# Kernel tuning notes

Hardware: AMD Instinct MI355X
Metric: run time of the kernel (lower is better)

The kernel has to match this reference:

```python
import jax, jax.numpy as jnp
import numpy as np

B, P, K = 8, 1024, 20  # clouds, points per cloud, kNN neighbors
OUT = 40
EPS = 1e-5


def leaky(x):
    return jnp.where(x >= 0, x, 0.2 * x)


def batch_norm(h, gamma, beta):
    mu = jnp.mean(h, axis=0)
    var = jnp.var(h, axis=0)
    return (h - mu) * jax.lax.rsqrt(var + EPS) * gamma + beta


def edge_conv(x, W, b, k):
    # x: [B,P,C]. Dynamic kNN in feature space (self included, as torch_cluster knn),
    # edge feature nn([x_i, x_j - x_i]) (single plain Linear per PyG MLP plain_last),
    # then max-aggregation over the k neighbors.
    sq = jnp.sum(x * x, axis=-1)                                  # [B,P]
    d = sq[:, :, None] + sq[:, None, :] - 2.0 * jnp.einsum('bpc,bqc->bpq', x, x)
    idx = jax.lax.top_k(-d, k)[1]                                  # [B,P,k]
    xj = jax.vmap(lambda xc, ic: xc[ic])(x, idx)                   # [B,P,k,C]
    xi = jnp.broadcast_to(x[:, :, None, :], xj.shape)
    e = jnp.concatenate([xi, xj - xi], axis=-1)                    # [B,P,k,2C]
    h = jnp.einsum('bpke,ec->bpkc', e, W) + b
    return jnp.max(h, axis=2)                                      # [B,P,Cout]


def setup_inputs() -> dict:
    key = jax.random.key(0)
    ks = jax.random.split(key, 16)
    s = 0.1
    pos = jax.random.normal(ks[0], (B * P, 3), dtype=jnp.float32)
    batch = jnp.repeat(jnp.arange(B, dtype=jnp.int32), P)
    return {
        'pos': pos, 'batch': batch,
        'W1': jax.random.normal(ks[1], (6, 64), jnp.float32) * s,    'b1': jnp.zeros((64,), jnp.float32),
        'W2': jax.random.normal(ks[2], (128, 64), jnp.float32) * s,  'b2': jnp.zeros((64,), jnp.float32),
        'W3': jax.random.normal(ks[3], (128, 128), jnp.float32) * s, 'b3': jnp.zeros((128,), jnp.float32),
        'W4': jax.random.normal(ks[4], (256, 256), jnp.float32) * s, 'b4': jnp.zeros((256,), jnp.float32),
        'Wm': jax.random.normal(ks[5], (512, 1024), jnp.float32) * s, 'bm': jnp.zeros((1024,), jnp.float32),
        'Wa': jax.random.normal(ks[6], (2048, 512), jnp.float32) * s, 'ba': jnp.zeros((512,), jnp.float32),
        'ga': jnp.ones((512,), jnp.float32),  'bea': jnp.zeros((512,), jnp.float32),
        'Wb': jax.random.normal(ks[7], (512, 256), jnp.float32) * s, 'bb': jnp.zeros((256,), jnp.float32),
        'gb': jnp.ones((256,), jnp.float32),  'beb': jnp.zeros((256,), jnp.float32),
        'Wc': jax.random.normal(ks[8], (256, OUT), jnp.float32) * s, 'bc': jnp.zeros((OUT,), jnp.float32),
    }


def reference(pos, batch, W1, b1, W2, b2, W3, b3, W4, b4, Wm, bm,
              Wa, ba, ga, bea, Wb, bb, gb, beb, Wc, bc):
    # batch ids are contiguous with P points per cloud -> reshape to [B,P,.]
    x = pos.reshape(B, P, 3)
    x1 = edge_conv(x, W1, b1, K)    # [B,P,64]
    x2 = edge_conv(x1, W2, b2, K)   # [B,P,64]
    x3 = edge_conv(x2, W3, b3, K)   # [B,P,128]
    x4 = edge_conv(x3, W4, b4, K)   # [B,P,256]
    cat = jnp.concatenate([x1, x2, x3, x4], axis=-1)  # [B,P,512]
    out = cat @ Wm + bm                                # [B,P,1024] (plain Linear)
    gmax = jnp.max(out, axis=1)                        # global_max_pool  [B,1024]
    gmean = jnp.mean(out, axis=1)                      # global_mean_pool [B,1024]
    h = jnp.concatenate([gmax, gmean], axis=-1)        # [B,2048]
    h = leaky(batch_norm(h @ Wa + ba, ga, bea))        # dropout = identity (eval)
    h = leaky(batch_norm(h @ Wb + bb, gb, beb))
    return h @ Wc + bc                                 # [B,40]
```

## Files before the change

kernel.cpp:

```cpp
#include <hip/hip_runtime.h>
#include <hip/hip_bf16.h>

#define NB 8
#define NP 1024
#define NPTS (NB * NP)
#define KNN 20

using bf16x8 = __attribute__((ext_vector_type(8))) short;
using f32x4 = __attribute__((ext_vector_type(4))) float;
using u64x16 = __attribute__((ext_vector_type(16))) unsigned long long;
using u32x16 = __attribute__((ext_vector_type(16))) unsigned int;

static __device__ __forceinline__ unsigned long long umin64(unsigned long long a,
                                                            unsigned long long b) {
    return a < b ? a : b;
}

static __device__ __forceinline__ void split_bf16(float v, unsigned short& h,
                                                  unsigned short& l) {
    __hip_bfloat16 hb = __float2bfloat16(v);
    float hf = __bfloat162float(hb);
    __hip_bfloat16 lb = __float2bfloat16(v - hf);
    h = *(unsigned short*)&hb;
    l = *(unsigned short*)&lb;
// ... 44 lines not shown
        if (r == KNN - 1) break;
        unsigned mlo = (unsigned)m;
#pragma unroll
        for (int j = 0; j < 16; ++j)
            if ((unsigned)k[j] == mlo) k[j] = ~0ull;
    }
}

static __device__ __forceinline__ void topk20_sel(u32x16 d, int lane,
                                                  unsigned long long* __restrict__ cand,
                                                  int* __restrict__ out) {
    unsigned lm = d[0];
#pragma unroll
    for (int j = 1; j < 16; ++j) lm = (d[j] < lm) ? d[j] : lm;
    unsigned srt = wave_bitonic_sort_u32(lm, lane);
    unsigned T = (unsigned)__shfl((int)srt, 19, 64);

    const unsigned long long below = (1ull << lane) - 1ull;
    int base = 0;
#pragma unroll
    for (int j = 0; j < 16; ++j) {
        bool sel = (d[j] <= T);
        unsigned long long mask = __ballot(sel);
        if (sel) {
            int pos = base + (int)__popcll(mask & below);
            if (pos < 64)
                cand[pos] = ((unsigned long long)d[j] << 32) | (unsigned)(j * 64 + lane);
        }
        base += (int)__popcll(mask);
    }

    if (base <= 64) {
        unsigned long long v = (lane < base) ? cand[lane] : ~0ull;
        unsigned hi = (unsigned)(v >> 32);
        unsigned hs = wave_bitonic_sort_u32(hi, lane);
        unsigned t2 = (unsigned)__shfl((int)hs, 19, 64);
        bool sel2 = (lane < base) && (hi <= t2);
        unsigned long long m2 = __ballot(sel2);
        if ((int)__popcll(m2) == KNN) {
            if (sel2) out[(int)__popcll(m2 & below)] = (int)(v & 0xffffffffu);
        } else {
            unsigned long long sv = wave_bitonic_sort(v, lane);
            if (lane < KNN) out[lane] = (int)(sv & 0xffffffffu);
        }
    } else {
        u64x16 k;
#pragma unroll
        for (int j = 0; j < 16; ++j)
            k[j] = ((unsigned long long)d[j] << 32) | (unsigned)(j * 64 + lane);
        topk20_wave(k, lane, out);
    }
}

__global__ __launch_bounds__(256) void knn3_kernel(const float* __restrict__ x,
                                                   int* __restrict__ idx) {
    const int w = threadIdx.x >> 6, lane = threadIdx.x & 63;
    const int p = blockIdx.x * 4 + w;
    const int b = p >> 10, pr = p & 1023;
    const int tid = threadIdx.x;
    __shared__ float sx[3][1024];
    __shared__ float ssq[1024];
    __shared__ unsigned long long cand[4][64];
    const float* xb = x + (size_t)b * NP * 3;

    for (int t = tid; t < 1024; t += 256) {
        float vx = xb[t * 3 + 0], vy = xb[t * 3 + 1], vz = xb[t * 3 + 2];
        sx[0][t] = vx;
        sx[1][t] = vy;
        sx[2][t] = vz;
        ssq[t] = vx * vx + vy * vy + vz * vz;
    }
    __syncthreads();

    const float px = sx[0][pr], py = sx[1][pr], pz = sx[2][pr];
    const float sqp = ssq[pr];

    u32x16 d;
#pragma unroll
    for (int j = 0; j < 16; ++j) {
        int q = j * 64 + lane;
        float dot = px * sx[0][q];
        dot += py * sx[1][q];
        dot += pz * sx[2][q];
        float dv = sqp + ssq[q] - 2.0f * dot;
        unsigned u = __float_as_uint(dv);
        d[j] = (u & 0x80000000u) ? ~u : (u | 0x80000000u);
    }
    topk20_sel(d, lane, cand[w], idx + (size_t)p * KNN);
}

template <int C>
__global__ __launch_bounds__(256) void sqnorm_kernel(const float* __restrict__ x,
                                                     float* __restrict__ sqn) {
    int p = blockIdx.x * 256 + threadIdx.x;
    if (p < NPTS) {
        const float* xp = x + (size_t)p * C;
        float s = 0.f;
        for (int c = 0; c < C; ++c) s += xp[c] * xp[c];
        sqn[p] = s;
    }
}

static __device__ __forceinline__ void pack_store(unsigned short h[8],
                                                  unsigned short l[8], size_t ci,
                                                  unsigned short* __restrict__ Wh,
                                                  unsigned short* __restrict__ Wl) {
    uint4 hp, lp;
    hp.x = h[0] | ((unsigned)h[1] << 16);
    hp.y = h[2] | ((unsigned)h[3] << 16);
    hp.z = h[4] | ((unsigned)h[5] << 16);
    hp.w = h[6] | ((unsigned)h[7] << 16);
    lp.x = l[0] | ((unsigned)l[1] << 16);
    lp.y = l[2] | ((unsigned)l[3] << 16);
    lp.z = l[4] | ((unsigned)l[5] << 16);
    lp.w = l[6] | ((unsigned)l[7] << 16);
    ((uint4*)Wh)[ci] = hp;
    ((uint4*)Wl)[ci] = lp;
}

static __device__ void conv_edge_w(const float* __restrict__ W, int Cin, int Cout,
                                   int g, unsigned short* __restrict__ Wh,
                                   unsigned short* __restrict__ Wl) {
    int N2 = 2 * Cout;
    if (g >= (Cin / 8) * N2) return;
    int n = g % N2, ks = g / N2;
    unsigned short h[8], l[8];
#pragma unroll
    for (int j = 0; j < 8; ++j) {
        int c = ks * 8 + j;
        float v;
        if (n < Cout)
            v = W[(size_t)c * Cout + n] - W[(size_t)(Cin + c) * Cout + n];
        else
            v = W[(size_t)(Cin + c) * Cout + (n - Cout)];
        split_bf16(v, h[j], l[j]);
    }
    pack_store(h, l, (size_t)ks * N2 + n, Wh, Wl);
}

__global__ __launch_bounds__(256) void convert_all_w_kernel(
        const float* __restrict__ Wm, const float* __restrict__ W2,
        const float* __restrict__ W3, const float* __restrict__ W4,
        unsigned short* __restrict__ Wmh, unsigned short* __restrict__ Wml,
        unsigned short* __restrict__ W2h, unsigned short* __restrict__ W2l,
        unsigned short* __restrict__ W3h, unsigned short* __restrict__ W3l,
        unsigned short* __restrict__ W4h, unsigned short* __restrict__ W4l) {
    int bid = blockIdx.x;
    if (bid < 256) {
        int g = bid * 256 + threadIdx.x;
        int n = g & 1023, ks = g >> 10;
        unsigned short h[8], l[8];
#pragma unroll
        for (int j = 0; j < 8; ++j) {
            float v = Wm[(size_t)(ks * 8 + j) * 1024 + n];
            split_bf16(v, h[j], l[j]);
        }
        pack_store(h, l, (size_t)ks * 1024 + n, Wmh, Wml);
    } else if (bid < 288) {
        conv_edge_w(W4, 128, 256, (bid - 256) * 256 + threadIdx.x, W4h, W4l);
    } else if (bid < 296) {
        conv_edge_w(W3, 64, 128, (bid - 288) * 256 + threadIdx.x, W3h, W3l);
    } else {
        conv_edge_w(W2, 64, 64, (bid - 296) * 256 + threadIdx.x, W2h, W2l);
    }
}

template <int C>
__global__ __launch_bounds__(256, 2) void knn_mfma_kernel(
        const unsigned short* __restrict__ Xhp, const unsigned short* __restrict__ Xlp,
        const float* __restrict__ sqn, int* __restrict__ idx) {
    constexpr int NCK = C / 32;
    const int bid = blockIdx.x;
    const int b = bid >> 6, rg = bid & 63;
    const int g0 = b * NP;
    const int p0 = rg * 16;
    const int tid = threadIdx.x;
    const int wid = tid >> 6, lane = tid & 63;
    const int fkb = lane >> 4, flm = lane & 15;

    __shared__ float sD[16][1028];
    __shared__ float sqa[16];
    __shared__ float sqb[1024];
    __shared__ unsigned long long cand[4][64];

    if (tid < 16) sqa[tid] = sqn[g0 + p0 + tid];
    for (int t = tid; t < 1024; t += 256) sqb[t] = sqn[g0 + t];
    __syncthreads();

    const uint4* Ah4 = (const uint4*)Xhp;
    const uint4* Al4 = (const uint4*)Xlp;

    uint4 fAh[NCK], fAl[NCK];
#pragma unroll
    for (int kk = 0; kk < NCK; ++kk) {
        size_t a = (size_t)(4 * kk + fkb) * NPTS + g0 + p0 + flm;
        fAh[kk] = Ah4[a];
        fAl[kk] = Al4[a];
    }

    const int r4 = fkb * 4, cc = flm;

#pragma unroll
    for (int t = 0; t < 2; ++t) {
        const int c0 = (wid + t * 4) * 128;
        f32x4 acc[8];
#pragma unroll
        for (int j = 0; j < 8; ++j) acc[j] = {0.f, 0.f, 0.f, 0.f};

#pragma unroll
        for (int kk = 0; kk < NCK; ++kk) {
            uint4 fBh[8], fBl[8];
#pragma unroll
            for (int j = 0; j < 8; ++j) {
                size_t bi = (size_t)(4 * kk + fkb) * NPTS + g0 + c0 + j * 16 + flm;
                fBh[j] = Ah4[bi];
                fBl[j] = Al4[bi];
            }
            bf16x8 ah = *(const bf16x8*)&fAh[kk];
            bf16x8 al = *(const bf16x8*)&fAl[kk];
#pragma unroll
            for (int j = 0; j < 8; ++j) {
                bf16x8 bh = *(const bf16x8*)&fBh[j];
                bf16x8 bl = *(const bf16x8*)&fBl[j];
                acc[j] = __builtin_amdgcn_mfma_f32_16x16x32_bf16(ah, bh, acc[j], 0, 0, 0);
                acc[j] = __builtin_amdgcn_mfma_f32_16x16x32_bf16(ah, bl, acc[j], 0, 0, 0);
                acc[j] = __builtin_amdgcn_mfma_f32_16x16x32_bf16(al, bh, acc[j], 0, 0, 0);
            }
        }

#pragma unroll
        for (int r = 0; r < 4; ++r) {
            int row = r4 + r;
            float sp = sqa[row];
#pragma unroll
            for (int j = 0; j < 8; ++j) {
                int col = c0 + j * 16 + cc;
                sD[row][col] = sp + sqb[col] - 2.0f * acc[j][r];
            }
        }
    }
    __syncthreads();

    for (int rr = 0; rr < 4; ++rr) {
        int row = wid * 4 + rr;
        u32x16 d;
#pragma unroll
        for (int j = 0; j < 16; ++j) {
            int q = j * 64 + lane;
            unsigned u = __float_as_uint(sD[row][q]);
            d[j] = (u & 0x80000000u) ? ~u : (u | 0x80000000u);
        }
        topk20_sel(d, lane, cand[wid], idx + (size_t)(g0 + p0 + row) * KNN);
    }
}

template <int Cin, int Cout>
__global__ __launch_bounds__(256, 2) void edge_mfma_kernel(
        const unsigned short* __restrict__ Xhp, const unsigned short* __restrict__ Xlp,
        const unsigned short* __restrict__ Whp, const unsigned short* __restrict__ Wlp,
        const float* __restrict__ bias, float* __restrict__ AB) {
    constexpr int N2 = 2 * Cout;
    constexpr int NCK = Cin / 32;
    const int n0 = blockIdx.x * 128;
    const int p0 = blockIdx.y * 128;
    const int tid = threadIdx.x;
    const int wid = tid >> 6, lane = tid & 63;
    const int wm = (wid >> 1) * 64, wn = (wid & 1) * 64;

    __shared__ uint4 sAh[2][4][132], sAl[2][4][132], sBh[2][4][132], sBl[2][4][132];

    f32x4 acc[4][4];
#pragma unroll
    for (int i = 0; i < 4; ++i)
#pragma unroll
        for (int j = 0; j < 4; ++j) acc[i][j] = {0.f, 0.f, 0.f, 0.f};

    const uint4* Ah4 = (const uint4*)Xhp;
    const uint4* Al4 = (const uint4*)Xlp;
    const uint4* Wh4 = (const uint4*)Whp;
    const uint4* Wl4 = (const uint4*)Wlp;

    const int m0 = tid & 127, kb0 = tid >> 7;
    uint4 rAh0, rAl0, rBh0, rBl0, rAh1, rAl1, rBh1, rBl1;

#define EM_LOAD(ck)                                                     \
    {                                                                   \
        int ksb = (ck) * 4;                                             \
        size_t a0 = (size_t)(ksb + kb0) * NPTS + p0 + m0;               \
        size_t a1 = (size_t)(ksb + kb0 + 2) * NPTS + p0 + m0;           \
        size_t b0 = (size_t)(ksb + kb0) * N2 + n0 + m0;                 \
        size_t b1 = (size_t)(ksb + kb0 + 2) * N2 + n0 + m0;             \
        rAh0 = Ah4[a0]; rAl0 = Al4[a0];                                 \
        rAh1 = Ah4[a1]; rAl1 = Al4[a1];                                 \
        rBh0 = Wh4[b0]; rBl0 = Wl4[b0];                                 \
        rBh1 = Wh4[b1]; rBl1 = Wl4[b1];                                 \
    }

#define EM_WRITE(buf)                                                   \
    {                                                                   \
        sAh[buf][kb0][m0] = rAh0;  sAl[buf][kb0][m0] = rAl0;            \
        sAh[buf][kb0 + 2][m0] = rAh1;  sAl[buf][kb0 + 2][m0] = rAl1;    \
        sBh[buf][kb0][m0] = rBh0;  sBl[buf][kb0][m0] = rBl0;            \
        sBh[buf][kb0 + 2][m0] = rBh1;  sBl[buf][kb0 + 2][m0] = rBl1;    \
    }

    EM_LOAD(0);
    EM_WRITE(0);
    __syncthreads();

    const int fkb = lane >> 4, flm = lane & 15;

    for (int ck = 0; ck < NCK; ++ck) {
        const int buf = ck & 1;
        if (ck < NCK - 1) EM_LOAD(ck + 1);

        bf16x8 fAh[4], fAl[4], fBh[4], fBl[4];
#pragma unroll
        for (int i = 0; i < 4; ++i) {
            fAh[i] = *(const bf16x8*)&sAh[buf][fkb][wm + i * 16 + flm];
            fAl[i] = *(const bf16x8*)&sAl[buf][fkb][wm + i * 16 + flm];
            fBh[i] = *(const bf16x8*)&sBh[buf][fkb][wn + i * 16 + flm];
            fBl[i] = *(const bf16x8*)&sBl[buf][fkb][wn + i * 16 + flm];
        }
#pragma unroll
        for (int i = 0; i < 4; ++i)
#pragma unroll
            for (int j = 0; j < 4; ++j) {
                acc[i][j] = __builtin_amdgcn_mfma_f32_16x16x32_bf16(fAh[i], fBh[j],
                                                                    acc[i][j], 0, 0, 0);
                acc[i][j] = __builtin_amdgcn_mfma_f32_16x16x32_bf16(fAh[i], fBl[j],
                                                                    acc[i][j], 0, 0, 0);
                acc[i][j] = __builtin_amdgcn_mfma_f32_16x16x32_bf16(fAl[i], fBh[j],
                                                                    acc[i][j], 0, 0, 0);
            }

        if (ck < NCK - 1) EM_WRITE(buf ^ 1);
        __syncthreads();
    }

    const int r4 = (lane >> 4) * 4, cc = lane & 15;
    float bj[4];
#pragma unroll
    for (int j = 0; j < 4; ++j) {
        int cg = n0 + wn + j * 16 + cc;
        bj[j] = (cg < Cout) ? bias[cg] : 0.f;
    }
#pragma unroll
    for (int i = 0; i < 4; ++i) {
#pragma unroll
        for (int r = 0; r < 4; ++r) {
            int row = wm + i * 16 + r4 + r;
            float* orow = AB + (size_t)(p0 + row) * N2 + n0;
#pragma unroll
            for (int j = 0; j < 4; ++j)
                orow[wn + j * 16 + cc] = acc[i][j][r] + bj[j];
        }
    }
#undef EM_LOAD
#undef EM_WRITE
}

template <int Cin, int Cout>
__global__ __launch_bounds__(256) void edge_gemm_kernel(const float* __restrict__ x,
                                                        const float* __restrict__ W,
                                                        const float* __restrict__ bias,
                                                        float* __restrict__ AB) {
    constexpr int N2 = 2 * Cout;
    constexpr int BK = (Cin < 32) ? Cin : 32;
    const int n0 = blockIdx.x * 128;
    const int p0 = blockIdx.y * 64;
    const int tid = threadIdx.x;
    const int tx = tid & 15, ty = tid >> 4;

    __shared__ float sX[BK][68];
    __shared__ float sW[BK][132];

    float acc[4][8];
#pragma unroll
    for (int i = 0; i < 4; ++i)
#pragma unroll
        for (int j = 0; j < 8; ++j) acc[i][j] = 0.f;

    for (int k0 = 0; k0 < Cin; k0 += BK) {
        for (int t = tid; t < 64 * BK; t += 256) {
            int m = t / BK, c = t - m * BK;
            sX[c][m] = x[(size_t)(p0 + m) * Cin + c];
        }
        for (int t = tid; t < BK * 128; t += 256) {
            int c = t >> 7, n = t & 127;
            int nn = n0 + n;
            float w;
            if (nn < Cout)
                w = W[(size_t)(k0 + c) * Cout + nn] - W[(size_t)(Cin + k0 + c) * Cout + nn];
            else
                w = W[(size_t)(Cin + k0 + c) * Cout + (nn - Cout)];
            sW[c][n] = w;
        }
        __syncthreads();

#pragma unroll
        for (int c = 0; c < BK; ++c) {
            float4 a4 = *(const float4*)&sX[c][ty * 4];
            float4 w0 = *(const float4*)&sW[c][tx * 4];
            float4 w1 = *(const float4*)&sW[c][64 + tx * 4];
            float av[4] = {a4.x, a4.y, a4.z, a4.w};
#pragma unroll
            for (int i = 0; i < 4; ++i) {
                acc[i][0] += av[i] * w0.x;
                acc[i][1] += av[i] * w0.y;
                acc[i][2] += av[i] * w0.z;
                acc[i][3] += av[i] * w0.w;
                acc[i][4] += av[i] * w1.x;
                acc[i][5] += av[i] * w1.y;
                acc[i][6] += av[i] * w1.z;
                acc[i][7] += av[i] * w1.w;
            }
        }
        __syncthreads();
    }

    const bool aH0 = (n0 < Cout);
    const bool aH1 = (n0 + 64 < Cout);
    float4 z4 = {0.f, 0.f, 0.f, 0.f};
    float4 bb0 = aH0 ? *(const float4*)&bias[n0 + tx * 4] : z4;
    float4 bb1 = aH1 ? *(const float4*)&bias[n0 + 64 + tx * 4] : z4;

#pragma unroll
    for (int i = 0; i < 4; ++i) {
        float* orow = AB + (size_t)(p0 + ty * 4 + i) * N2 + n0;
        float4 o0, o1;
        o0.x = acc[i][0] + bb0.x;
        o0.y = acc[i][1] + bb0.y;
        o0.z = acc[i][2] + bb0.z;
        o0.w = acc[i][3] + bb0.w;
        o1.x = acc[i][4] + bb1.x;
        o1.y = acc[i][5] + bb1.y;
        o1.z = acc[i][6] + bb1.z;
        o1.w = acc[i][7] + bb1.w;
        *(float4*)&orow[tx * 4] = o0;
        *(float4*)&orow[64 + tx * 4] = o1;
    }
}

template <int Cout>
__global__ __launch_bounds__(256) void gather_max_panel_kernel(
        const float* __restrict__ AB, const int* __restrict__ idx,
        float* __restrict__ y, unsigned short* __restrict__ Xh,
        unsigned short* __restrict__ Xl) {
    constexpr int N2 = 2 * Cout;
    constexpr int TPP = Cout / 4;
    constexpr int PPB = 256 / TPP;
    constexpr int RS = N2 / 4;
    const int pp = threadIdx.x / TPP;
    const int t = threadIdx.x % TPP;
    const int p = blockIdx.x * PPB + pp;
    const int base = p & ~(NP - 1);

    __shared__ int s_idx[PPB][KNN];
    for (int tt = threadIdx.x; tt < PPB * KNN; tt += 256) {
        int a = tt / KNN, r = tt - a * KNN;
        s_idx[a][r] = idx[(size_t)(blockIdx.x * PPB + a) * KNN + r];
    }
    __syncthreads();

    const float4* Brow = (const float4*)(AB + (size_t)base * N2 + Cout);

    int q0 = s_idx[pp][0];
    float4 m = Brow[(size_t)q0 * RS + t];
#pragma unroll
    for (int j = 1; j < KNN; ++j) {
        int q = s_idx[pp][j];
        float4 v = Brow[(size_t)q * RS + t];
        m.x = fmaxf(m.x, v.x);
        m.y = fmaxf(m.y, v.y);
        m.z = fmaxf(m.z, v.z);
        m.w = fmaxf(m.w, v.w);
    }
    float4 a = *(const float4*)(AB + (size_t)p * N2 + 4 * t);
    float4 o;
    o.x = a.x + m.x;
    o.y = a.y + m.y;
    o.z = a.z + m.z;
    o.w = a.w + m.w;
    *(float4*)(y + (size_t)p * Cout + 4 * t) = o;

    unsigned short h[4], l[4];
    split_bf16(o.x, h[0], l[0]);
    split_bf16(o.y, h[1], l[1]);
    split_bf16(o.z, h[2], l[2]);
    split_bf16(o.w, h[3], l[3]);
    const int ks = t >> 1;
    size_t u2 = ((size_t)ks * NPTS + p) * 2 + (t & 1);
    uint2 hp, lp;
    hp.x = h[0] | ((unsigned)h[1] << 16);
    hp.y = h[2] | ((unsigned)h[3] << 16);
    lp.x = l[0] | ((unsigned)l[1] << 16);
    lp.y = l[2] | ((unsigned)l[3] << 16);
    ((uint2*)Xh)[u2] = hp;
    ((uint2*)Xl)[u2] = lp;
}

__global__ __launch_bounds__(256) void catmean_kernel(
        const float* __restrict__ x1, const float* __restrict__ x2,
        const float* __restrict__ x3, const float* __restrict__ x4,
        float* __restrict__ catmean) {
    const int n0 = blockIdx.x * 128;
    const int b = blockIdx.y;
    const int tid = threadIdx.x;
    const int col = n0 + (tid & 127);
    const int half = tid >> 7;
    __shared__ float sred[256];

    const float* src;
    int cw, coff;
    if (col < 64) { src = x1; cw = 64; coff = col; }
    else if (col < 128) { src = x2; cw = 64; coff = col - 64; }
    else if (col < 256) { src = x3; cw = 128; coff = col - 128; }
    else { src = x4; cw = 256; coff = col - 256; }

    float s = 0.f;
    const float* base = src + ((size_t)b * NP + half * 512) * cw + coff;
    for (int p = 0; p < 512; ++p) s += base[(size_t)p * cw];
    sred[tid] = s;
    __syncthreads();
    if (tid < 128)
        catmean[(size_t)b * 512 + col] = (sred[tid] + sred[tid + 128]) * (1.0f / 1024.0f);
}

__global__ __launch_bounds__(256) void gmean_kernel(const float* __restrict__ catmean,
                                                    const float* __restrict__ Wm,
                                                    const float* __restrict__ bm,
                                                    float* __restrict__ gmeanv) {
    const int n0 = blockIdx.x * 128;
    const int b = blockIdx.y;
    const int tid = threadIdx.x;
    const int cg = tid & 31, kp = tid >> 5;
    const int col = n0 + cg * 4;
    __shared__ float4 part[8][32];

    float4 acc = {0.f, 0.f, 0.f, 0.f};
    for (int k = kp * 64; k < kp * 64 + 64; ++k) {
        float g = catmean[(size_t)b * 512 + k];
        float4 w = *(const float4*)&Wm[(size_t)k * 1024 + col];
        acc.x += g * w.x;
        acc.y += g * w.y;
        acc.z += g * w.z;
        acc.w += g * w.w;
    }
    part[kp][cg] = acc;
    __syncthreads();
    if (tid < 32) {
        float4 s = part[0][tid];
// ... 284 lines not shown
    const float* Wa = (const float*)d_in[12];
    const float* ba = (const float*)d_in[13];
    const float* ga = (const float*)d_in[14];
    const float* bea = (const float*)d_in[15];
    const float* Wb = (const float*)d_in[16];
    const float* bb = (const float*)d_in[17];
    const float* gb = (const float*)d_in[18];
    const float* beb = (const float*)d_in[19];
    const float* Wc = (const float*)d_in[20];
    const float* bc = (const float*)d_in[21];
    float* out = (float*)d_out;

    char* ws = (char*)d_ws;
    size_t off = 0;
    auto alloc = [&](size_t bytes) {
        void* p = ws + off;
        off += (bytes + 255) & ~(size_t)255;
        return p;
    };
    int* idx = (int*)alloc((size_t)NPTS * KNN * 4);
    float* x1 = (float*)alloc((size_t)NPTS * 64 * 4);
    float* x2 = (float*)alloc((size_t)NPTS * 64 * 4);
    float* x3 = (float*)alloc((size_t)NPTS * 128 * 4);
    float* x4 = (float*)alloc((size_t)NPTS * 256 * 4);
    float* scratch = (float*)alloc((size_t)NPTS * 512 * 4);
    float* pmax = (float*)alloc((size_t)64 * 1024 * 4);
    float* catmean = (float*)alloc(NB * 512 * 4);
    float* gmeanv = (float*)alloc(NB * 1024 * 4);
    float* ha = (float*)alloc(NB * 512 * 4);
    float* hb = (float*)alloc(NB * 256 * 4);
    float* sqn = (float*)alloc(NPTS * 4);
    unsigned short* Ach = (unsigned short*)alloc((size_t)64 * NPTS * 8 * 2);
    unsigned short* Acl = (unsigned short*)alloc((size_t)64 * NPTS * 8 * 2);
    unsigned short* Wth = (unsigned short*)alloc((size_t)64 * 1024 * 8 * 2);
    unsigned short* Wtl = (unsigned short*)alloc((size_t)64 * 1024 * 8 * 2);
    unsigned short* W2h = (unsigned short*)alloc((size_t)8 * 128 * 8 * 2);
    unsigned short* W2l = (unsigned short*)alloc((size_t)8 * 128 * 8 * 2);
    unsigned short* W3h = (unsigned short*)alloc((size_t)8 * 256 * 8 * 2);
    unsigned short* W3l = (unsigned short*)alloc((size_t)8 * 256 * 8 * 2);
    unsigned short* W4h = (unsigned short*)alloc((size_t)16 * 512 * 8 * 2);
    unsigned short* W4l = (unsigned short*)alloc((size_t)16 * 512 * 8 * 2);
    (void)ws_size;

    float* AB = scratch;
    const size_t REG = (size_t)NPTS * 8;
    unsigned short* x1h = Ach, *x1l = Acl;
    unsigned short* x2h = Ach + 8 * REG, *x2l = Acl + 8 * REG;
    unsigned short* x3h = Ach + 16 * REG, *x3l = Acl + 16 * REG;
    unsigned short* x4h = Ach + 32 * REG, *x4l = Acl + 32 * REG;

    convert_all_w_kernel<<<300, 256, 0, stream>>>(Wm, W2, W3, W4, Wth, Wtl, W2h, W2l,
                                                  W3h, W3l, W4h, W4l);

    knn3_kernel<<<NPTS / 4, 256, 0, stream>>>(pos, idx);
    edge_gemm_kernel<3, 64><<<dim3(1, 128), 256, 0, stream>>>(pos, W1, b1, AB);
    gather_max_panel_kernel<64><<<NPTS / 16, 256, 0, stream>>>(AB, idx, x1, x1h, x1l);

    sqnorm_kernel<64><<<NPTS / 256, 256, 0, stream>>>(x1, sqn);
    knn_mfma_kernel<64><<<512, 256, 0, stream>>>(x1h, x1l, sqn, idx);
    edge_mfma_kernel<64, 64><<<dim3(1, 64), 256, 0, stream>>>(x1h, x1l, W2h, W2l, b2, AB);
    gather_max_panel_kernel<64><<<NPTS / 16, 256, 0, stream>>>(AB, idx, x2, x2h, x2l);

    sqnorm_kernel<64><<<NPTS / 256, 256, 0, stream>>>(x2, sqn);
    knn_mfma_kernel<64><<<512, 256, 0, stream>>>(x2h, x2l, sqn, idx);
    edge_mfma_kernel<64, 128><<<dim3(2, 64), 256, 0, stream>>>(x2h, x2l, W3h, W3l, b3, AB);
    gather_max_panel_kernel<128><<<NPTS / 8, 256, 0, stream>>>(AB, idx, x3, x3h, x3l);

    sqnorm_kernel<128><<<NPTS / 256, 256, 0, stream>>>(x3, sqn);
    knn_mfma_kernel<128><<<512, 256, 0, stream>>>(x3h, x3l, sqn, idx);
    edge_mfma_kernel<128, 256><<<dim3(4, 64), 256, 0, stream>>>(x3h, x3l, W4h, W4l, b4, AB);
    gather_max_panel_kernel<256><<<NPTS / 4, 256, 0, stream>>>(AB, idx, x4, x4h, x4l);

    catmean_kernel<<<dim3(4, NB), 256, 0, stream>>>(x1, x2, x3, x4, catmean);
    gmean_kernel<<<dim3(8, NB), 256, 0, stream>>>(catmean, Wm, bm, gmeanv);

    gemm_cat_pool_kernel<<<512, 256, 0, stream>>>(Ach, Acl, Wth, Wtl, pmax);

    fc_a_kernel<<<dim3(8, NB), 256, 0, stream>>>(pmax, gmeanv, bm, Wa, ba, ha);
    fc_b_bn_kernel<<<dim3(4, NB), 256, 0, stream>>>(ha, ga, bea, Wb, bb, hb);
    fc_c_bn_kernel<<<2, 256, 0, stream>>>(hb, gb, beb, Wc, bc, out);
}
```

Baseline: 241.6 us.

## Fuse kNN and edge GEMM per layer into one launch, fold sqnorm into gather

Merges each layer's kNN kernel and its independent edge projection GEMM into a single launch, with block ID ranges picking the role and a shared-memory union between the two. The layer-1 kNN now handles 16 points per block instead of 4. The separate squared-norm kernels are folded into the gather-max kernel, which writes the norms from a shared row buffer. This removes several launches and lets the two independent workloads overlap on the GPU. The cost is a larger shared-memory footprint for the GEMM blocks and an extra barrier plus a serial per-point norm loop in the gather.

```diff
diff --git a/kernel.cpp b/kernel.cpp
--- a/kernel.cpp
+++ b/kernel.cpp
@@ -120,52 +120,397 @@
     }
 }
 
-__global__ __launch_bounds__(256) void knn3_kernel(const float* __restrict__ x,
-                                                   int* __restrict__ idx) {
-    const int w = threadIdx.x >> 6, lane = threadIdx.x & 63;
-    const int p = blockIdx.x * 4 + w;
-    const int b = p >> 10, pr = p & 1023;
+struct Knn3Shared {
+    float sx[3][1024];
+    float ssq[1024];
+    unsigned long long cand[4][64];
+};
+struct Edge1Shared {
+    float sX[3][68];
+    float sW[3][132];
+};
+union L1Shared {
+    Knn3Shared k;
+    Edge1Shared e;
+};
+
+struct KnnShared {
+    float sD[16][1028];
+    float sqa[16];
+    float sqb[1024];
+    unsigned long long cand[4][64];
+};
+struct EdgeShared {
+    uint4 sAh[2][4][132];
+    uint4 sAl[2][4][132];
+    uint4 sBh[2][4][132];
+    uint4 sBl[2][4][132];
+};
+union LayerShared {
+    KnnShared k;
+    EdgeShared e;
+};
+
+__global__ __launch_bounds__(256) void knn3_edge_kernel(const float* __restrict__ x,
+                                                        const float* __restrict__ W,
+                                                        const float* __restrict__ bias,
+                                                        int* __restrict__ idx,
+                                                        float* __restrict__ AB) {
+    __shared__ L1Shared su;
+    const int bid = blockIdx.x;
     const int tid = threadIdx.x;
-    __shared__ float sx[3][1024];
-    __shared__ float ssq[1024];
-    __shared__ unsigned long long cand[4][64];
-    const float* xb = x + (size_t)b * NP * 3;
-
-    for (int t = tid; t < 1024; t += 256) {
-        float vx = xb[t * 3 + 0], vy = xb[t * 3 + 1], vz = xb[t * 3 + 2];
-        sx[0][t] = vx;
-        sx[1][t] = vy;
-        sx[2][t] = vz;
-        ssq[t] = vx * vx + vy * vy + vz * vz;
-    }
-    __syncthreads();
-
-    const float px = sx[0][pr], py = sx[1][pr], pz = sx[2][pr];
-    const float sqp = ssq[pr];
-
-    u32x16 d;
-#pragma unroll
-    for (int j = 0; j < 16; ++j) {
-        int q = j * 64 + lane;
-        float dot = px * sx[0][q];
-        dot += py * sx[1][q];
-        dot += pz * sx[2][q];
-        float dv = sqp + ssq[q] - 2.0f * dot;
-        unsigned u = __float_as_uint(dv);
-        d[j] = (u & 0x80000000u) ? ~u : (u | 0x80000000u);
-    }
-    topk20_sel(d, lane, cand[w], idx + (size_t)p * KNN);
-}
-
-template <int C>
-__global__ __launch_bounds__(256) void sqnorm_kernel(const float* __restrict__ x,
-                                                     float* __restrict__ sqn) {
-    int p = blockIdx.x * 256 + threadIdx.x;
-    if (p < NPTS) {
-        const float* xp = x + (size_t)p * C;
-        float s = 0.f;
-        for (int c = 0; c < C; ++c) s += xp[c] * xp[c];
-        sqn[p] = s;
+
+    if (bid < 512) {
+        Knn3Shared& S = su.k;
+        const int wid = tid >> 6, lane = tid & 63;
+        const int b = bid >> 6, p0 = (bid & 63) * 16;
+        const int g0 = b * NP;
+        const float* xb = x + (size_t)g0 * 3;
+
+        for (int t = tid; t < 1024; t += 256) {
+            float vx = xb[t * 3 + 0], vy = xb[t * 3 + 1], vz = xb[t * 3 + 2];
+            S.sx[0][t] = vx;
+            S.sx[1][t] = vy;
+            S.sx[2][t] = vz;
+            S.ssq[t] = vx * vx + vy * vy + vz * vz;
+        }
+        __syncthreads();
+
+        for (int rr = 0; rr < 4; ++rr) {
+            int pr = p0 + wid * 4 + rr;
+            const float px = S.sx[0][pr], py = S.sx[1][pr], pz = S.sx[2][pr];
+            const float sqp = S.ssq[pr];
+            u32x16 d;
+#pragma unroll
+            for (int j = 0; j < 16; ++j) {
+                int q = j * 64 + lane;
+                float dot = px * S.sx[0][q];
+                dot += py * S.sx[1][q];
+                dot += pz * S.sx[2][q];
+                float dv = sqp + S.ssq[q] - 2.0f * dot;
+                unsigned u = __float_as_uint(dv);
+                d[j] = (u & 0x80000000u) ? ~u : (u | 0x80000000u);
+            }
+            topk20_sel(d, lane, S.cand[wid], idx + (size_t)(g0 + pr) * KNN);
+        }
+    } else {
+        Edge1Shared& S = su.e;
+        constexpr int Cin = 3, Cout = 64, N2 = 128;
+        const int p0 = (bid - 512) * 64;
+        const int tx = tid & 15, ty = tid >> 4;
+
+        for (int t = tid; t < 64 * Cin; t += 256) {
+            int m = t / Cin, c = t - m * Cin;
+            S.sX[c][m] = x[(size_t)(p0 + m) * Cin + c];
+        }
+        for (int t = tid; t < Cin * 128; t += 256) {
+            int c = t >> 7, n = t & 127;
+            float w;
+            if (n < Cout)
+                w = W[(size_t)c * Cout + n] - W[(size_t)(Cin + c) * Cout + n];
+            else
+                w = W[(size_t)(Cin + c) * Cout + (n - Cout)];
+            S.sW[c][n] = w;
+        }
+        __syncthreads();
+
+        float acc[4][8];
+#pragma unroll
+        for (int i = 0; i < 4; ++i)
+#pragma unroll
+            for (int j = 0; j < 8; ++j) acc[i][j] = 0.f;
+
+#pragma unroll
+        for (int c = 0; c < Cin; ++c) {
+            float4 a4 = *(const float4*)&S.sX[c][ty * 4];
+            float4 w0 = *(const float4*)&S.sW[c][tx * 4];
+            float4 w1 = *(const float4*)&S.sW[c][64 + tx * 4];
+            float av[4] = {a4.x, a4.y, a4.z, a4.w};
+#pragma unroll
+            for (int i = 0; i < 4; ++i) {
+                acc[i][0] += av[i] * w0.x;
+                acc[i][1] += av[i] * w0.y;
+                acc[i][2] += av[i] * w0.z;
+                acc[i][3] += av[i] * w0.w;
+                acc[i][4] += av[i] * w1.x;
+                acc[i][5] += av[i] * w1.y;
+                acc[i][6] += av[i] * w1.z;
+                acc[i][7] += av[i] * w1.w;
+            }
+        }
+
+        float4 bb0 = *(const float4*)&bias[tx * 4];
+#pragma unroll
+        for (int i = 0; i < 4; ++i) {
+            float* orow = AB + (size_t)(p0 + ty * 4 + i) * N2;
+            float4 o0, o1;
+            o0.x = acc[i][0] + bb0.x;
+            o0.y = acc[i][1] + bb0.y;
+            o0.z = acc[i][2] + bb0.z;
+            o0.w = acc[i][3] + bb0.w;
+            o1.x = acc[i][4];
+            o1.y = acc[i][5];
+            o1.z = acc[i][6];
+            o1.w = acc[i][7];
+            *(float4*)&orow[tx * 4] = o0;
+            *(float4*)&orow[64 + tx * 4] = o1;
+        }
+    }
+}
+
+template <int C, int Cout>
+__global__ __launch_bounds__(256, 2) void layer_kernel(
+        const unsigned short* __restrict__ Xhp, const unsigned short* __restrict__ Xlp,
+        const float* __restrict__ sqn, int* __restrict__ idx,
+        const unsigned short* __restrict__ Whp, const unsigned short* __restrict__ Wlp,
+        const float* __restrict__ bias, float* __restrict__ AB) {
+    __shared__ LayerShared su;
+    constexpr int NCK = C / 32;
+    const int bid = blockIdx.x;
+    const int tid = threadIdx.x;
+    const int wid = tid >> 6, lane = tid & 63;
+    const int fkb = lane >> 4, flm = lane & 15;
+    const uint4* Ah4 = (const uint4*)Xhp;
+    const uint4* Al4 = (const uint4*)Xlp;
+
+    if (bid < 512) {
+        KnnShared& S = su.k;
+        const int b = bid >> 6, rg = bid & 63;
+        const int g0 = b * NP;
+        const int p0 = rg * 16;
+
+        if (tid < 16) S.sqa[tid] = sqn[g0 + p0 + tid];
+        for (int t = tid; t < 1024; t += 256) S.sqb[t] = sqn[g0 + t];
+        __syncthreads();
+
+        uint4 fAh[NCK], fAl[NCK];
+#pragma unroll
+        for (int kk = 0; kk < NCK; ++kk) {
+            size_t a = (size_t)(4 * kk + fkb) * NPTS + g0 + p0 + flm;
+            fAh[kk] = Ah4[a];
+            fAl[kk] = Al4[a];
+        }
+
+        const int r4 = fkb * 4, cc = flm;
+
+#pragma unroll
+        for (int t = 0; t < 2; ++t) {
+            const int c0 = (wid + t * 4) * 128;
+            f32x4 acc[8];
+#pragma unroll
+            for (int j = 0; j < 8; ++j) acc[j] = {0.f, 0.f, 0.f, 0.f};
+
+#pragma unroll
+            for (int kk = 0; kk < NCK; ++kk) {
+                uint4 fBh[8], fBl[8];
+#pragma unroll
+                for (int j = 0; j < 8; ++j) {
+                    size_t bi = (size_t)(4 * kk + fkb) * NPTS + g0 + c0 + j * 16 + flm;
+                    fBh[j] = Ah4[bi];
+                    fBl[j] = Al4[bi];
+                }
+                bf16x8 ah = *(const bf16x8*)&fAh[kk];
+                bf16x8 al = *(const bf16x8*)&fAl[kk];
+#pragma unroll
+                for (int j = 0; j < 8; ++j) {
+                    bf16x8 bh = *(const bf16x8*)&fBh[j];
+                    bf16x8 bl = *(const bf16x8*)&fBl[j];
+                    acc[j] = __builtin_amdgcn_mfma_f32_16x16x32_bf16(ah, bh, acc[j], 0, 0, 0);
+                    acc[j] = __builtin_amdgcn_mfma_f32_16x16x32_bf16(ah, bl, acc[j], 0, 0, 0);
+                    acc[j] = __builtin_amdgcn_mfma_f32_16x16x32_bf16(al, bh, acc[j], 0, 0, 0);
+                }
+            }
+
+#pragma unroll
+            for (int r = 0; r < 4; ++r) {
+                int row = r4 + r;
+                float sp = S.sqa[row];
+#pragma unroll
+                for (int j = 0; j < 8; ++j) {
+                    int col = c0 + j * 16 + cc;
+                    S.sD[row][col] = sp + S.sqb[col] - 2.0f * acc[j][r];
+                }
+            }
+        }
+        __syncthreads();
+
+        for (int rr = 0; rr < 4; ++rr) {
+            int row = wid * 4 + rr;
+            u32x16 d;
+#pragma unroll
+            for (int j = 0; j < 16; ++j) {
+                int q = j * 64 + lane;
+                unsigned u = __float_as_uint(S.sD[row][q]);
+                d[j] = (u & 0x80000000u) ? ~u : (u | 0x80000000u);
+            }
+            topk20_sel(d, lane, S.cand[wid], idx + (size_t)(g0 + p0 + row) * KNN);
+        }
+    } else {
+        EdgeShared& S = su.e;
+        constexpr int N2 = 2 * Cout;
+        constexpr int NX = N2 / 128;
+        const int eb = bid - 512;
+        const int n0 = (eb % NX) * 128;
+        const int p0 = (eb / NX) * 128;
+        const int wm = (wid >> 1) * 64, wn = (wid & 1) * 64;
+
+        f32x4 acc[4][4];
+#pragma unroll
+        for (int i = 0; i < 4; ++i)
+#pragma unroll
+            for (int j = 0; j < 4; ++j) acc[i][j] = {0.f, 0.f, 0.f, 0.f};
+
+        const uint4* Wh4 = (const uint4*)Whp;
+        const uint4* Wl4 = (const uint4*)Wlp;
+
+        const int m0 = tid & 127, kb0 = tid >> 7;
+        uint4 rAh0, rAl0, rBh0, rBl0, rAh1, rAl1, rBh1, rBl1;
+
+#define EM_LOAD(ck)                                                     \
+    {                                                                   \
+        int ksb = (ck) * 4;                                             \
+        size_t a0 = (size_t)(ksb + kb0) * NPTS + p0 + m0;               \
+        size_t a1 = (size_t)(ksb + kb0 + 2) * NPTS + p0 + m0;           \
+        size_t b0 = (size_t)(ksb + kb0) * N2 + n0 + m0;                 \
+        size_t b1 = (size_t)(ksb + kb0 + 2) * N2 + n0 + m0;             \
+        rAh0 = Ah4[a0]; rAl0 = Al4[a0];                                 \
+        rAh1 = Ah4[a1]; rAl1 = Al4[a1];                                 \
+        rBh0 = Wh4[b0]; rBl0 = Wl4[b0];                                 \
+        rBh1 = Wh4[b1]; rBl1 = Wl4[b1];                                 \
+    }
+
+#define EM_WRITE(buf)                                                         \
+    {                                                                         \
+        S.sAh[buf][kb0][m0] = rAh0;  S.sAl[buf][kb0][m0] = rAl0;              \
+        S.sAh[buf][kb0 + 2][m0] = rAh1;  S.sAl[buf][kb0 + 2][m0] = rAl1;      \
+        S.sBh[buf][kb0][m0] = rBh0;  S.sBl[buf][kb0][m0] = rBl0;              \
+        S.sBh[buf][kb0 + 2][m0] = rBh1;  S.sBl[buf][kb0 + 2][m0] = rBl1;      \
+    }
+
+        EM_LOAD(0);
+        EM_WRITE(0);
+        __syncthreads();
+
+        for (int ck = 0; ck < NCK; ++ck) {
+            const int buf = ck & 1;
+            if (ck < NCK - 1) EM_LOAD(ck + 1);
+
+            bf16x8 fAh[4], fAl[4], fBh[4], fBl[4];
+#pragma unroll
+            for (int i = 0; i < 4; ++i) {
+                fAh[i] = *(const bf16x8*)&S.sAh[buf][fkb][wm + i * 16 + flm];
+                fAl[i] = *(const bf16x8*)&S.sAl[buf][fkb][wm + i * 16 + flm];
+                fBh[i] = *(const bf16x8*)&S.sBh[buf][fkb][wn + i * 16 + flm];
+                fBl[i] = *(const bf16x8*)&S.sBl[buf][fkb][wn + i * 16 + flm];
+            }
+#pragma unroll
+            for (int i = 0; i < 4; ++i)
+#pragma unroll
+                for (int j = 0; j < 4; ++j) {
+                    acc[i][j] = __builtin_amdgcn_mfma_f32_16x16x32_bf16(
+                            fAh[i], fBh[j], acc[i][j], 0, 0, 0);
+                    acc[i][j] = __builtin_amdgcn_mfma_f32_16x16x32_bf16(
+                            fAh[i], fBl[j], acc[i][j], 0, 0, 0);
+                    acc[i][j] = __builtin_amdgcn_mfma_f32_16x16x32_bf16(
+                            fAl[i], fBh[j], acc[i][j], 0, 0, 0);
+                }
+
+            if (ck < NCK - 1) EM_WRITE(buf ^ 1);
+            __syncthreads();
+        }
+
+        const int r4 = (lane >> 4) * 4, cc = lane & 15;
+        float bj[4];
+#pragma unroll
+        for (int j = 0; j < 4; ++j) {
+            int cg = n0 + wn + j * 16 + cc;
+            bj[j] = (cg < Cout) ? bias[cg] : 0.f;
+        }
+#pragma unroll
+        for (int i = 0; i < 4; ++i) {
+#pragma unroll
+            for (int r = 0; r < 4; ++r) {
+                int row = wm + i * 16 + r4 + r;
+                float* orow = AB + (size_t)(p0 + row) * N2 + n0;
+#pragma unroll
+                for (int j = 0; j < 4; ++j)
+                    orow[wn + j * 16 + cc] = acc[i][j][r] + bj[j];
+            }
+        }
+#undef EM_LOAD
+#undef EM_WRITE
+    }
+}
+
+template <int Cout, bool WSQ>
+__global__ __launch_bounds__(256) void gather_max_panel_kernel(
+        const float* __restrict__ AB, const int* __restrict__ idx,
+        float* __restrict__ y, unsigned short* __restrict__ Xh,
+        unsigned short* __restrict__ Xl, float* __restrict__ sqn) {
+    constexpr int N2 = 2 * Cout;
+    constexpr int TPP = Cout / 4;
+    constexpr int PPB = 256 / TPP;
+    constexpr int RS = N2 / 4;
+    const int pp = threadIdx.x / TPP;
+    const int t = threadIdx.x % TPP;
+    const int p = blockIdx.x * PPB + pp;
+    const int base = p & ~(NP - 1);
+
+    __shared__ int s_idx[PPB][KNN];
+    __shared__ float srow[PPB][Cout];
+    for (int tt = threadIdx.x; tt < PPB * KNN; tt += 256) {
+        int a = tt / KNN, r = tt - a * KNN;
+        s_idx[a][r] = idx[(size_t)(blockIdx.x * PPB + a) * KNN + r];
+    }
+    __syncthreads();
+
+    const float4* Brow = (const float4*)(AB + (size_t)base * N2 + Cout);
+
+    int q0 = s_idx[pp][0];
+    float4 m = Brow[(size_t)q0 * RS + t];
+#pragma unroll
+    for (int j = 1; j < KNN; ++j) {
+        int q = s_idx[pp][j];
+        float4 v = Brow[(size_t)q * RS + t];
+        m.x = fmaxf(m.x, v.x);
+        m.y = fmaxf(m.y, v.y);
+        m.z = fmaxf(m.z, v.z);
+        m.w = fmaxf(m.w, v.w);
+    }
+    float4 a = *(const float4*)(AB + (size_t)p * N2 + 4 * t);
+    float4 o;
+    o.x = a.x + m.x;
+    o.y = a.y + m.y;
+    o.z = a.z + m.z;
+    o.w = a.w + m.w;
+    *(float4*)(y + (size_t)p * Cout + 4 * t) = o;
+
+    unsigned short h[4], l[4];
+    split_bf16(o.x, h[0], l[0]);
+    split_bf16(o.y, h[1], l[1]);
+    split_bf16(o.z, h[2], l[2]);
+    split_bf16(o.w, h[3], l[3]);
+    const int ks = t >> 1;
+    size_t u2 = ((size_t)ks * NPTS + p) * 2 + (t & 1);
+    uint2 hp, lp;
+    hp.x = h[0] | ((unsigned)h[1] << 16);
+    hp.y = h[2] | ((unsigned)h[3] << 16);
+    lp.x = l[0] | ((unsigned)l[1] << 16);
+    lp.y = l[2] | ((unsigned)l[3] << 16);
+    ((uint2*)Xh)[u2] = hp;
+    ((uint2*)Xl)[u2] = lp;
+
+    if constexpr (WSQ) {
+        *(float4*)&srow[pp][4 * t] = o;
+        __syncthreads();
+        if (t == 0) {
+            float s = 0.f;
+            for (int c = 0; c < Cout; ++c) {
+                float v = srow[pp][c];
+                s += v * v;
+            }
+            sqn[p] = s;
+        }
     }
 }
 
@@ -231,341 +576,6 @@
     } else {
         conv_edge_w(W2, 64, 64, (bid - 296) * 256 + threadIdx.x, W2h, W2l);
     }
-}
-
-template <int C>
-__global__ __launch_bounds__(256, 2) void knn_mfma_kernel(
-        const unsigned short* __restrict__ Xhp, const unsigned short* __restrict__ Xlp,
-        const float* __restrict__ sqn, int* __restrict__ idx) {
-    constexpr int NCK = C / 32;
-    const int bid = blockIdx.x;
-    const int b = bid >> 6, rg = bid & 63;
-    const int g0 = b * NP;
-    const int p0 = rg * 16;
-    const int tid = threadIdx.x;
-    const int wid = tid >> 6, lane = tid & 63;
-    const int fkb = lane >> 4, flm = lane & 15;
-
-    __shared__ float sD[16][1028];
-    __shared__ float sqa[16];
-    __shared__ float sqb[1024];
-    __shared__ unsigned long long cand[4][64];
-
-    if (tid < 16) sqa[tid] = sqn[g0 + p0 + tid];
-    for (int t = tid; t < 1024; t += 256) sqb[t] = sqn[g0 + t];
-    __syncthreads();
-
-    const uint4* Ah4 = (const uint4*)Xhp;
-    const uint4* Al4 = (const uint4*)Xlp;
-
-    uint4 fAh[NCK], fAl[NCK];
-#pragma unroll
-    for (int kk = 0; kk < NCK; ++kk) {
-        size_t a = (size_t)(4 * kk + fkb) * NPTS + g0 + p0 + flm;
-        fAh[kk] = Ah4[a];
-        fAl[kk] = Al4[a];
-    }
-
-    const int r4 = fkb * 4, cc = flm;
-
-#pragma unroll
-    for (int t = 0; t < 2; ++t) {
-        const int c0 = (wid + t * 4) * 128;
-        f32x4 acc[8];
-#pragma unroll
-        for (int j = 0; j < 8; ++j) acc[j] = {0.f, 0.f, 0.f, 0.f};
-
-#pragma unroll
-        for (int kk = 0; kk < NCK; ++kk) {
-            uint4 fBh[8], fBl[8];
-#pragma unroll
-            for (int j = 0; j < 8; ++j) {
-                size_t bi = (size_t)(4 * kk + fkb) * NPTS + g0 + c0 + j * 16 + flm;
-                fBh[j] = Ah4[bi];
-                fBl[j] = Al4[bi];
-            }
-            bf16x8 ah = *(const bf16x8*)&fAh[kk];
-            bf16x8 al = *(const bf16x8*)&fAl[kk];
-#pragma unroll
-            for (int j = 0; j < 8; ++j) {
-                bf16x8 bh = *(const bf16x8*)&fBh[j];
-                bf16x8 bl = *(const bf16x8*)&fBl[j];
-                acc[j] = __builtin_amdgcn_mfma_f32_16x16x32_bf16(ah, bh, acc[j], 0, 0, 0);
-                acc[j] = __builtin_amdgcn_mfma_f32_16x16x32_bf16(ah, bl, acc[j], 0, 0, 0);
-                acc[j] = __builtin_amdgcn_mfma_f32_16x16x32_bf16(al, bh, acc[j], 0, 0, 0);
-            }
-        }
-
-#pragma unroll
-        for (int r = 0; r < 4; ++r) {
-            int row = r4 + r;
-            float sp = sqa[row];
-#pragma unroll
-            for (int j = 0; j < 8; ++j) {
-                int col = c0 + j * 16 + cc;
-                sD[row][col] = sp + sqb[col] - 2.0f * acc[j][r];
-            }
-        }
-    }
-    __syncthreads();
-
-    for (int rr = 0; rr < 4; ++rr) {
-        int row = wid * 4 + rr;
-        u32x16 d;
-#pragma unroll
-        for (int j = 0; j < 16; ++j) {
-            int q = j * 64 + lane;
-            unsigned u = __float_as_uint(sD[row][q]);
-            d[j] = (u & 0x80000000u) ? ~u : (u | 0x80000000u);
-        }
-        topk20_sel(d, lane, cand[wid], idx + (size_t)(g0 + p0 + row) * KNN);
-    }
-}
-
-template <int Cin, int Cout>
-__global__ __launch_bounds__(256, 2) void edge_mfma_kernel(
-        const unsigned short* __restrict__ Xhp, const unsigned short* __restrict__ Xlp,
-        const unsigned short* __restrict__ Whp, const unsigned short* __restrict__ Wlp,
-        const float* __restrict__ bias, float* __restrict__ AB) {
-    constexpr int N2 = 2 * Cout;
-    constexpr int NCK = Cin / 32;
-    const int n0 = blockIdx.x * 128;
-    const int p0 = blockIdx.y * 128;
-    const int tid = threadIdx.x;
-    const int wid = tid >> 6, lane = tid & 63;
-    const int wm = (wid >> 1) * 64, wn = (wid & 1) * 64;
-
-    __shared__ uint4 sAh[2][4][132], sAl[2][4][132], sBh[2][4][132], sBl[2][4][132];
-
-    f32x4 acc[4][4];
-#pragma unroll
-    for (int i = 0; i < 4; ++i)
-#pragma unroll
-        for (int j = 0; j < 4; ++j) acc[i][j] = {0.f, 0.f, 0.f, 0.f};
-
-    const uint4* Ah4 = (const uint4*)Xhp;
-    const uint4* Al4 = (const uint4*)Xlp;
-    const uint4* Wh4 = (const uint4*)Whp;
-    const uint4* Wl4 = (const uint4*)Wlp;
-
-    const int m0 = tid & 127, kb0 = tid >> 7;
-    uint4 rAh0, rAl0, rBh0, rBl0, rAh1, rAl1, rBh1, rBl1;
-
-#define EM_LOAD(ck)                                                     \
-    {                                                                   \
-        int ksb = (ck) * 4;                                             \
-        size_t a0 = (size_t)(ksb + kb0) * NPTS + p0 + m0;               \
-        size_t a1 = (size_t)(ksb + kb0 + 2) * NPTS + p0 + m0;           \
-        size_t b0 = (size_t)(ksb + kb0) * N2 + n0 + m0;                 \
-        size_t b1 = (size_t)(ksb + kb0 + 2) * N2 + n0 + m0;             \
-        rAh0 = Ah4[a0]; rAl0 = Al4[a0];                                 \
-        rAh1 = Ah4[a1]; rAl1 = Al4[a1];                                 \
-        rBh0 = Wh4[b0]; rBl0 = Wl4[b0];                                 \
-        rBh1 = Wh4[b1]; rBl1 = Wl4[b1];                                 \
-    }
-
-#define EM_WRITE(buf)                                                   \
-    {                                                                   \
-        sAh[buf][kb0][m0] = rAh0;  sAl[buf][kb0][m0] = rAl0;            \
-        sAh[buf][kb0 + 2][m0] = rAh1;  sAl[buf][kb0 + 2][m0] = rAl1;    \
-        sBh[buf][kb0][m0] = rBh0;  sBl[buf][kb0][m0] = rBl0;            \
-        sBh[buf][kb0 + 2][m0] = rBh1;  sBl[buf][kb0 + 2][m0] = rBl1;    \
-    }
-
-    EM_LOAD(0);
-    EM_WRITE(0);
-    __syncthreads();
-
-    const int fkb = lane >> 4, flm = lane & 15;
-
-    for (int ck = 0; ck < NCK; ++ck) {
-        const int buf = ck & 1;
-        if (ck < NCK - 1) EM_LOAD(ck + 1);
-
-        bf16x8 fAh[4], fAl[4], fBh[4], fBl[4];
-#pragma unroll
-        for (int i = 0; i < 4; ++i) {
-            fAh[i] = *(const bf16x8*)&sAh[buf][fkb][wm + i * 16 + flm];
-            fAl[i] = *(const bf16x8*)&sAl[buf][fkb][wm + i * 16 + flm];
-            fBh[i] = *(const bf16x8*)&sBh[buf][fkb][wn + i * 16 + flm];
-            fBl[i] = *(const bf16x8*)&sBl[buf][fkb][wn + i * 16 + flm];
-        }
-#pragma unroll
-        for (int i = 0; i < 4; ++i)
-#pragma unroll
-            for (int j = 0; j < 4; ++j) {
-                acc[i][j] = __builtin_amdgcn_mfma_f32_16x16x32_bf16(fAh[i], fBh[j],
-                                                                    acc[i][j], 0, 0, 0);
-                acc[i][j] = __builtin_amdgcn_mfma_f32_16x16x32_bf16(fAh[i], fBl[j],
-                                                                    acc[i][j], 0, 0, 0);
-                acc[i][j] = __builtin_amdgcn_mfma_f32_16x16x32_bf16(fAl[i], fBh[j],
-                                                                    acc[i][j], 0, 0, 0);
-            }
-
-        if (ck < NCK - 1) EM_WRITE(buf ^ 1);
-        __syncthreads();
-    }
-
-    const int r4 = (lane >> 4) * 4, cc = lane & 15;
-    float bj[4];
-#pragma unroll
-    for (int j = 0; j < 4; ++j) {
-        int cg = n0 + wn + j * 16 + cc;
-        bj[j] = (cg < Cout) ? bias[cg] : 0.f;
-    }
-#pragma unroll
-    for (int i = 0; i < 4; ++i) {
-#pragma unroll
-        for (int r = 0; r < 4; ++r) {
-            int row = wm + i * 16 + r4 + r;
-            float* orow = AB + (size_t)(p0 + row) * N2 + n0;
-#pragma unroll
-            for (int j = 0; j < 4; ++j)
-                orow[wn + j * 16 + cc] = acc[i][j][r] + bj[j];
-        }
-    }
-#undef EM_LOAD
-#undef EM_WRITE
-}
-
-template <int Cin, int Cout>
-__global__ __launch_bounds__(256) void edge_gemm_kernel(const float* __restrict__ x,
-                                                        const float* __restrict__ W,
-                                                        const float* __restrict__ bias,
-                                                        float* __restrict__ AB) {
-    constexpr int N2 = 2 * Cout;
-    constexpr int BK = (Cin < 32) ? Cin : 32;
-    const int n0 = blockIdx.x * 128;
-    const int p0 = blockIdx.y * 64;
-    const int tid = threadIdx.x;
-    const int tx = tid & 15, ty = tid >> 4;
-
-    __shared__ float sX[BK][68];
-    __shared__ float sW[BK][132];
-
-    float acc[4][8];
-#pragma unroll
-    for (int i = 0; i < 4; ++i)
-#pragma unroll
-        for (int j = 0; j < 8; ++j) acc[i][j] = 0.f;
-
-    for (int k0 = 0; k0 < Cin; k0 += BK) {
-        for (int t = tid; t < 64 * BK; t += 256) {
-            int m = t / BK, c = t - m * BK;
-            sX[c][m] = x[(size_t)(p0 + m) * Cin + c];
-        }
-        for (int t = tid; t < BK * 128; t += 256) {
-            int c = t >> 7, n = t & 127;
-            int nn = n0 + n;
-            float w;
-            if (nn < Cout)
-                w = W[(size_t)(k0 + c) * Cout + nn] - W[(size_t)(Cin + k0 + c) * Cout + nn];
-            else
-                w = W[(size_t)(Cin + k0 + c) * Cout + (nn - Cout)];
-            sW[c][n] = w;
-        }
-        __syncthreads();
-
-#pragma unroll
-        for (int c = 0; c < BK; ++c) {
-            float4 a4 = *(const float4*)&sX[c][ty * 4];
-            float4 w0 = *(const float4*)&sW[c][tx * 4];
-            float4 w1 = *(const float4*)&sW[c][64 + tx * 4];
-            float av[4] = {a4.x, a4.y, a4.z, a4.w};
-#pragma unroll
-            for (int i = 0; i < 4; ++i) {
-                acc[i][0] += av[i] * w0.x;
-                acc[i][1] += av[i] * w0.y;
-                acc[i][2] += av[i] * w0.z;
-                acc[i][3] += av[i] * w0.w;
-                acc[i][4] += av[i] * w1.x;
-                acc[i][5] += av[i] * w1.y;
-                acc[i][6] += av[i] * w1.z;
-                acc[i][7] += av[i] * w1.w;
-            }
-        }
-        __syncthreads();
-    }
-
-    const bool aH0 = (n0 < Cout);
-    const bool aH1 = (n0 + 64 < Cout);
-    float4 z4 = {0.f, 0.f, 0.f, 0.f};
-    float4 bb0 = aH0 ? *(const float4*)&bias[n0 + tx * 4] : z4;
-    float4 bb1 = aH1 ? *(const float4*)&bias[n0 + 64 + tx * 4] : z4;
-
-#pragma unroll
-    for (int i = 0; i < 4; ++i) {
-        float* orow = AB + (size_t)(p0 + ty * 4 + i) * N2 + n0;
-        float4 o0, o1;
-        o0.x = acc[i][0] + bb0.x;
-        o0.y = acc[i][1] + bb0.y;
-        o0.z = acc[i][2] + bb0.z;
-        o0.w = acc[i][3] + bb0.w;
-        o1.x = acc[i][4] + bb1.x;
-        o1.y = acc[i][5] + bb1.y;
-        o1.z = acc[i][6] + bb1.z;
-        o1.w = acc[i][7] + bb1.w;
-        *(float4*)&orow[tx * 4] = o0;
-        *(float4*)&orow[64 + tx * 4] = o1;
-    }
-}
-
-template <int Cout>
-__global__ __launch_bounds__(256) void gather_max_panel_kernel(
-        const float* __restrict__ AB, const int* __restrict__ idx,
-        float* __restrict__ y, unsigned short* __restrict__ Xh,
-        unsigned short* __restrict__ Xl) {
-    constexpr int N2 = 2 * Cout;
-    constexpr int TPP = Cout / 4;
-    constexpr int PPB = 256 / TPP;
-    constexpr int RS = N2 / 4;
-    const int pp = threadIdx.x / TPP;
-    const int t = threadIdx.x % TPP;
-    const int p = blockIdx.x * PPB + pp;
-    const int base = p & ~(NP - 1);
-
-    __shared__ int s_idx[PPB][KNN];
-    for (int tt = threadIdx.x; tt < PPB * KNN; tt += 256) {
-        int a = tt / KNN, r = tt - a * KNN;
-        s_idx[a][r] = idx[(size_t)(blockIdx.x * PPB + a) * KNN + r];
-    }
-    __syncthreads();
-
-    const float4* Brow = (const float4*)(AB + (size_t)base * N2 + Cout);
-
-    int q0 = s_idx[pp][0];
-    float4 m = Brow[(size_t)q0 * RS + t];
-#pragma unroll
-    for (int j = 1; j < KNN; ++j) {
-        int q = s_idx[pp][j];
-        float4 v = Brow[(size_t)q * RS + t];
-        m.x = fmaxf(m.x, v.x);
-        m.y = fmaxf(m.y, v.y);
-        m.z = fmaxf(m.z, v.z);
-        m.w = fmaxf(m.w, v.w);
-    }
-    float4 a = *(const float4*)(AB + (size_t)p * N2 + 4 * t);
-    float4 o;
-    o.x = a.x + m.x;
-    o.y = a.y + m.y;
-    o.z = a.z + m.z;
-    o.w = a.w + m.w;
-    *(float4*)(y + (size_t)p * Cout + 4 * t) = o;
-
-    unsigned short h[4], l[4];
-    split_bf16(o.x, h[0], l[0]);
-    split_bf16(o.y, h[1], l[1]);
-    split_bf16(o.z, h[2], l[2]);
-    split_bf16(o.w, h[3], l[3]);
-    const int ks = t >> 1;
-    size_t u2 = ((size_t)ks * NPTS + p) * 2 + (t & 1);
-    uint2 hp, lp;
-    hp.x = h[0] | ((unsigned)h[1] << 16);
-    hp.y = h[2] | ((unsigned)h[3] << 16);
-    lp.x = l[0] | ((unsigned)l[1] << 16);
-    lp.y = l[2] | ((unsigned)l[3] << 16);
-    ((uint2*)Xh)[u2] = hp;
-    ((uint2*)Xl)[u2] = lp;
 }
 
 __global__ __launch_bounds__(256) void catmean_kernel(
@@ -956,24 +966,24 @@
     convert_all_w_kernel<<<300, 256, 0, stream>>>(Wm, W2, W3, W4, Wth, Wtl, W2h, W2l,
                                                   W3h, W3l, W4h, W4l);
 
-    knn3_kernel<<<NPTS / 4, 256, 0, stream>>>(pos, idx);
-    edge_gemm_kernel<3, 64><<<dim3(1, 128), 256, 0, stream>>>(pos, W1, b1, AB);
-    gather_max_panel_kernel<64><<<NPTS / 16, 256, 0, stream>>>(AB, idx, x1, x1h, x1l);
-
-    sqnorm_kernel<64><<<NPTS / 256, 256, 0, stream>>>(x1, sqn);
-    knn_mfma_kernel<64><<<512, 256, 0, stream>>>(x1h, x1l, sqn, idx);
-    edge_mfma_kernel<64, 64><<<dim3(1, 64), 256, 0, stream>>>(x1h, x1l, W2h, W2l, b2, AB);
-    gather_max_panel_kernel<64><<<NPTS / 16, 256, 0, stream>>>(AB, idx, x2, x2h, x2l);
-
-    sqnorm_kernel<64><<<NPTS / 256, 256, 0, stream>>>(x2, sqn);
-    knn_mfma_kernel<64><<<512, 256, 0, stream>>>(x2h, x2l, sqn, idx);
-    edge_mfma_kernel<64, 128><<<dim3(2, 64), 256, 0, stream>>>(x2h, x2l, W3h, W3l, b3, AB);
-    gather_max_panel_kernel<128><<<NPTS / 8, 256, 0, stream>>>(AB, idx, x3, x3h, x3l);
-
-    sqnorm_kernel<128><<<NPTS / 256, 256, 0, stream>>>(x3, sqn);
-    knn_mfma_kernel<128><<<512, 256, 0, stream>>>(x3h, x3l, sqn, idx);
-    edge_mfma_kernel<128, 256><<<dim3(4, 64), 256, 0, stream>>>(x3h, x3l, W4h, W4l, b4, AB);
-    gather_max_panel_kernel<256><<<NPTS / 4, 256, 0, stream>>>(AB, idx, x4, x4h, x4l);
+    knn3_edge_kernel<<<640, 256, 0, stream>>>(pos, W1, b1, idx, AB);
+    gather_max_panel_kernel<64, true><<<NPTS / 16, 256, 0, stream>>>(AB, idx, x1, x1h,
+                                                                     x1l, sqn);
+
+    layer_kernel<64, 64><<<512 + 64, 256, 0, stream>>>(x1h, x1l, sqn, idx, W2h, W2l,
+                                                       b2, AB);
+    gather_max_panel_kernel<64, true><<<NPTS / 16, 256, 0, stream>>>(AB, idx, x2, x2h,
+                                                                     x2l, sqn);
+
+    layer_kernel<64, 128><<<512 + 128, 256, 0, stream>>>(x2h, x2l, sqn, idx, W3h, W3l,
+                                                         b3, AB);
+    gather_max_panel_kernel<128, true><<<NPTS / 8, 256, 0, stream>>>(AB, idx, x3, x3h,
+                                                                     x3l, sqn);
+
+    layer_kernel<128, 256><<<512 + 256, 256, 0, stream>>>(x3h, x3l, sqn, idx, W4h, W4l,
+                                                          b4, AB);
+    gather_max_panel_kernel<256, false><<<NPTS / 4, 256, 0, stream>>>(AB, idx, x4, x4h,
+                                                                      x4l, nullptr);
 
     catmean_kernel<<<dim3(4, NB), 256, 0, stream>>>(x1, x2, x3, x4, catmean);
     gmean_kernel<<<dim3(8, NB), 256, 0, stream>>>(catmean, Wm, bm, gmeanv);
```

Result: faster. 222.2 us (-8.0%).
